# Optimization experiments

Measured on AMD Instinct MI355X. Metric: run time of the kernel, lower is better.

## Reference

```python
import jax, jax.numpy as jnp
import numpy as np

N_NODES = 50000
N_EDGES = 1600000
IN_DIM = 128
OUT_DIM = 64
HEADS = 4


def setup_inputs() -> dict:
    key = jax.random.key(0)
    k1, k2, k3, k4 = jax.random.split(key, 4)
    x = jax.random.normal(k1, (N_NODES, IN_DIM), dtype=jnp.float32)
    edge_index = jax.random.randint(k2, (2, N_EDGES), 0, N_NODES, dtype=jnp.int64)
    # W[h]: per-head linear weight (in_dim -> out_dim), no bias
    W = jax.random.normal(k3, (HEADS, IN_DIM, OUT_DIM), dtype=jnp.float32) * 0.1
    # a[h]: attention vector over concat([h_src, h_dst]) -> scalar, no bias
    a = jax.random.normal(k4, (HEADS, 2 * OUT_DIM), dtype=jnp.float32) * 0.1
    return {"x": x, "edge_index": edge_index, "W": W, "a": a}


def reference(x, edge_index, W, a):
    n_nodes = x.shape[0]
    out_dim = W.shape[2]
    src, dst = edge_index[0], edge_index[1]
    # per-head projection: [N, H, O]
    h = jnp.einsum('nf,hfo->nho', x, W)
    h_src = h[src]  # [E, H, O]
    h_dst = h[dst]  # [E, H, O]
    a_src, a_dst = a[:, :out_dim], a[:, out_dim:]  # split of concat weight
    # e = leaky_relu(a^T [h_src || h_dst]) per edge, per head: [E, H]
    e = jnp.einsum('eho,ho->eh', h_src, a_src) + jnp.einsum('eho,ho->eh', h_dst, a_dst)
    e = jax.nn.leaky_relu(e, negative_slope=0.01)
    # NOTE: faithful to source — softmax over ALL edges (dim=0), not per-dst
    alpha = jax.nn.softmax(e, axis=0)  # [E, H]
    msgs = h_src * alpha[:, :, None]  # [E, H, O]
    agg = jax.ops.segment_sum(msgs, dst, num_segments=n_nodes)  # [N, H, O]
    # concat heads along feature dim (head-major), matching torch.cat(out, dim=1)
    return agg.reshape(n_nodes, -1)
```

## Files before the change

### kernel.cpp

```cpp
#include <hip/hip_runtime.h>
#include <stdint.h>

#define N_NODES 50000
#define N_EDGES 1600000
#define IN_DIM  128
#define OUT_DIM 64
#define HEADS   4
#define HO      (HEADS*OUT_DIM)

typedef __attribute__((ext_vector_type(8))) short short8;
typedef __attribute__((ext_vector_type(8))) unsigned short bf16x8;
typedef __attribute__((ext_vector_type(4))) float f32x4;

__device__ __forceinline__ float lrelu(float v) {
    return v >= 0.f ? v : 0.01f * v;
}
__device__ __forceinline__ unsigned short f2bf(float f) {
    unsigned u = __float_as_uint(f);
    return (unsigned short)((u + 0x7FFFu + ((u >> 16) & 1u)) >> 16);
}
__device__ __forceinline__ float bf2f(unsigned short b) {
    return __uint_as_float(((unsigned)b) << 16);
}

__global__ __launch_bounds__(256) void k_prep_wt(
    const float* __restrict__ W, unsigned short* __restrict__ wt)
{
    int item = blockIdx.x * 256 + threadIdx.x;
    int n  = item >> 5;
    int k0 = (item & 31) * 4;
    int h = n >> 6, o = n & 63;
    const float* wp = &W[((size_t)h * IN_DIM + k0) * OUT_DIM + o];
    ushort4 u;
    u.x = f2bf(wp[0 * OUT_DIM]);
    u.y = f2bf(wp[1 * OUT_DIM]);
    u.z = f2bf(wp[2 * OUT_DIM]);
    u.w = f2bf(wp[3 * OUT_DIM]);
    *(ushort4*)&wt[(size_t)n * IN_DIM + k0] = u;
}

#define HIST_BLOCKS 1024
#define BM 64
#define GEMM_BLOCKS ((N_NODES + BM - 1) / BM)

__global__ __launch_bounds__(256) void k_gemm_hist(
    const float* __restrict__ x, const unsigned short* __restrict__ wt,
    const float* __restrict__ a, const int* __restrict__ edst,
    int* __restrict__ cnt, int* __restrict__ rank,
    unsigned short* __restrict__ hb, float* __restrict__ s_src, float* __restrict__ s_dst)
{
    extern __shared__ char smem[];

    if (blockIdx.x < HIST_BLOCKS) {
        const int stride = HIST_BLOCKS * 256;
        for (int e = blockIdx.x * 256 + threadIdx.x; e < N_EDGES; e += stride)
            rank[e] = atomicAdd(&cnt[edst[e]], 1);
        return;
    }

    char* Alds = smem;
    char* Blds = smem + 16384;

    const int tid  = threadIdx.x;
    const int wave = tid >> 6;
    const int lane = tid & 63;
    const int node0 = (blockIdx.x - HIST_BLOCKS) * BM;

    {
        #pragma unroll
        for (int j = 0; j < 4; ++j) {
            int o    = (j * 256 + tid) * 16;
            int row  = o >> 8;
            int fcol = (o & 255) >> 1;
            int node = node0 + row;
            const float* sp = x + (size_t)(node < N_NODES ? node : N_NODES - 1) * IN_DIM + fcol;
            float4 v0 = *(const float4*)sp;
            float4 v1 = *(const float4*)(sp + 4);
            bf16x8 u;
            u[0] = f2bf(v0.x); u[1] = f2bf(v0.y); u[2] = f2bf(v0.z); u[3] = f2bf(v0.w);
            u[4] = f2bf(v1.x); u[5] = f2bf(v1.y); u[6] = f2bf(v1.z); u[7] = f2bf(v1.w);
            int sw = o ^ (((o >> 8) & 7) << 4);
            *(bf16x8*)(Alds + sw) = u;
        }
    }
    {
        const char* wsrc = (const char*)wt;
        #pragma unroll
        for (int j = 0; j < 16; ++j) {
            int o = (j * 256 + tid) * 16;
            uint4 v = *(const uint4*)(wsrc + o);
            int sw = o ^ (((o >> 8) & 7) << 4);
            *(uint4*)(Blds + sw) = v;
        }
    }
    __syncthreads();

    const int wr0  = wave * 16;
    const int l15  = lane & 15;
    const int lhi  = lane >> 4;
    const int kxor = (lane & 7) << 4;

    short8 af[4];
    #pragma unroll
    for (int s = 0; s < 4; ++s)
        af[s] = *(const short8*)(Alds + (wr0 + l15) * 256 + ((s * 64 + lhi * 16) ^ kxor));

    f32x4 acc[16];
    #pragma unroll
    for (int nt = 0; nt < 16; ++nt) acc[nt] = (f32x4){0.f, 0.f, 0.f, 0.f};

    #pragma unroll
    for (int nt = 0; nt < 16; ++nt) {
        const char* bbase = Blds + (nt * 16 + l15) * 256;
        #pragma unroll
        for (int s = 0; s < 4; ++s) {
            short8 bf = *(const short8*)(bbase + ((s * 64 + lhi * 16) ^ kxor));
            acc[nt] = __builtin_amdgcn_mfma_f32_16x16x32_bf16(af[s], bf, acc[nt], 0, 0, 0);
        }
    }

    #pragma unroll
    for (int nt = 0; nt < 16; ++nt) {
        int col = nt * 16 + l15;
        #pragma unroll
        for (int r = 0; r < 4; ++r) {
            int node = node0 + wr0 + lhi * 4 + r;
            if (node < N_NODES)
                hb[(size_t)node * HO + col] = f2bf(acc[nt][r]);
        }
    }

    #pragma unroll
    for (int h = 0; h < 4; ++h) {
        float avs0 = a[h*128 +  0 + l15], avs1 = a[h*128 + 16 + l15];
        float avs2 = a[h*128 + 32 + l15], avs3 = a[h*128 + 48 + l15];
        float avd0 = a[h*128 + 64 + l15], avd1 = a[h*128 + 80 + l15];
        float avd2 = a[h*128 + 96 + l15], avd3 = a[h*128 + 112 + l15];
        #pragma unroll
        for (int r = 0; r < 4; ++r) {
            float vs = acc[4*h+0][r]*avs0 + acc[4*h+1][r]*avs1
                     + acc[4*h+2][r]*avs2 + acc[4*h+3][r]*avs3;
            float vd = acc[4*h+0][r]*avd0 + acc[4*h+1][r]*avd1
                     + acc[4*h+2][r]*avd2 + acc[4*h+3][r]*avd3;
            #pragma unroll
            for (int m = 8; m >= 1; m >>= 1) {
                vs += __shfl_xor(vs, m);
                vd += __shfl_xor(vd, m);
            }
            int node = node0 + wr0 + lhi * 4 + r;
            if (l15 == 0 && node < N_NODES) {
                s_src[node * HEADS + h] = vs;
                s_dst[node * HEADS + h] = vd;
            }
        }
    }
}

__global__ __launch_bounds__(1024) void k_mid(
    const int* __restrict__ cnt, int* __restrict__ row_start,
    const float* __restrict__ s_src, const float* __restrict__ s_dst,
    float* __restrict__ gmax)
{
    if (blockIdx.x == 0) {
        __shared__ int part[1024];
        const int t  = threadIdx.x;
        const int CH = (N_NODES + 1023) / 1024;
        const int lo = t * CH;
        const int hi = (lo + CH < N_NODES) ? lo + CH : N_NODES;

        int s = 0;
        for (int i = lo; i < hi; ++i) s += cnt[i];
        part[t] = s;
        __syncthreads();

        for (int off = 1; off < 1024; off <<= 1) {
            int v = (t >= off) ? part[t - off] : 0;
            __syncthreads();
            part[t] += v;
            __syncthreads();
        }

        int run = (t == 0) ? 0 : part[t - 1];
        for (int i = lo; i < hi; ++i) {
            row_start[i] = run;
            run += cnt[i];
        }
        if (t == 1023) row_start[N_NODES] = part[1023];
        return;
    }

    __shared__ float red[16][8];
    float4 ms = make_float4(-1e30f, -1e30f, -1e30f, -1e30f);
    float4 md = ms;
    for (int n = threadIdx.x; n < N_NODES; n += 1024) {
        float4 vs = ((const float4*)s_src)[n];
        float4 vd = ((const float4*)s_dst)[n];
        ms.x = fmaxf(ms.x, vs.x); ms.y = fmaxf(ms.y, vs.y);
        ms.z = fmaxf(ms.z, vs.z); ms.w = fmaxf(ms.w, vs.w);
        md.x = fmaxf(md.x, vd.x); md.y = fmaxf(md.y, vd.y);
        md.z = fmaxf(md.z, vd.z); md.w = fmaxf(md.w, vd.w);
    }
    #pragma unroll
    for (int m = 32; m >= 1; m >>= 1) {
        ms.x = fmaxf(ms.x, __shfl_xor(ms.x, m)); ms.y = fmaxf(ms.y, __shfl_xor(ms.y, m));
        ms.z = fmaxf(ms.z, __shfl_xor(ms.z, m)); ms.w = fmaxf(ms.w, __shfl_xor(ms.w, m));
        md.x = fmaxf(md.x, __shfl_xor(md.x, m)); md.y = fmaxf(md.y, __shfl_xor(md.y, m));
        md.z = fmaxf(md.z, __shfl_xor(md.z, m)); md.w = fmaxf(md.w, __shfl_xor(md.w, m));
    }
    const int w = threadIdx.x >> 6;
    if ((threadIdx.x & 63) == 0) {
        red[w][0] = ms.x; red[w][1] = ms.y; red[w][2] = ms.z; red[w][3] = ms.w;
        red[w][4] = md.x; red[w][5] = md.y; red[w][6] = md.z; red[w][7] = md.w;
    }
    __syncthreads();
    if (threadIdx.x < 8) {
        float m = red[0][threadIdx.x];
        #pragma unroll
        for (int k = 1; k < 16; ++k) m = fmaxf(m, red[k][threadIdx.x]);
        gmax[threadIdx.x] = m;
    }
}

#define BUCKET_BLOCKS 256
__global__ __launch_bounds__(256) void k_bucket(
    const int* __restrict__ esrc, const int* __restrict__ edst,
    const int* __restrict__ rank, const int* __restrict__ row_start,
    const float* __restrict__ s_src, const float* __restrict__ s_dst,
    const float* __restrict__ gmax,
    unsigned* __restrict__ rec, double* __restrict__ gsum)
{
    const float mx0 = lrelu(gmax[0] + gmax[4]);
    const float mx1 = lrelu(gmax[1] + gmax[5]);
    const float mx2 = lrelu(gmax[2] + gmax[6]);
    const float mx3 = lrelu(gmax[3] + gmax[7]);
    double a0 = 0.0, a1 = 0.0, a2 = 0.0, a3 = 0.0;
    const int stride = gridDim.x * blockDim.x;
    for (int e = blockIdx.x * blockDim.x + threadIdx.x; e < N_EDGES; e += stride) {
        int s = esrc[e], d = edst[e];
        int pos = row_start[d] + rank[e];
        float4 ss = *(const float4*)&s_src[s * HEADS];
        float4 sd = *(const float4*)&s_dst[d * HEADS];
        unsigned b0 = f2bf(__expf(lrelu(ss.x + sd.x) - mx0));
        unsigned b1 = f2bf(__expf(lrelu(ss.y + sd.y) - mx1));
        unsigned b2 = f2bf(__expf(lrelu(ss.z + sd.z) - mx2));
        unsigned b3 = f2bf(__expf(lrelu(ss.w + sd.w) - mx3));
        rec[(size_t)pos * 3 + 0] = (unsigned)s;
        rec[(size_t)pos * 3 + 1] = b0 | (b1 << 16);
        rec[(size_t)pos * 3 + 2] = b2 | (b3 << 16);
        a0 += (double)bf2f((unsigned short)b0);
        a1 += (double)bf2f((unsigned short)b1);
        a2 += (double)bf2f((unsigned short)b2);
        a3 += (double)bf2f((unsigned short)b3);
    }
    #pragma unroll
    for (int m = 32; m >= 1; m >>= 1) {
        a0 += __shfl_xor(a0, m); a1 += __shfl_xor(a1, m);
        a2 += __shfl_xor(a2, m); a3 += __shfl_xor(a3, m);
    }
    __shared__ double part[4][4];
    const int wave = threadIdx.x >> 6;
    if ((threadIdx.x & 63) == 0) {
        part[wave][0] = a0; part[wave][1] = a1; part[wave][2] = a2; part[wave][3] = a3;
    }
    __syncthreads();
    if (threadIdx.x < 4) {
        double t = part[0][threadIdx.x] + part[1][threadIdx.x]
                 + part[2][threadIdx.x] + part[3][threadIdx.x];
        atomicAdd(&gsum[(blockIdx.x & 7) * 4 + threadIdx.x], t);
    }
}

__global__ __launch_bounds__(256) void k_agg(
    const int* __restrict__ row_start, const unsigned* __restrict__ rec,
    const unsigned short* __restrict__ hb,
    const double* __restrict__ gsum, float* __restrict__ out)
{
    const int wid = (int)((blockIdx.x * 256u + threadIdx.x) >> 6);
    if (wid >= N_NODES) return;
    const int lane = threadIdx.x & 63;
    const int half = lane >> 5;
    const int l32  = lane & 31;
    const int head = l32 >> 3;
    const int og   = (l32 & 7) * 8;
    const int hoff = head * OUT_DIM + og;

    const int beg = row_start[wid];
    const int end = row_start[wid + 1];
    double gs = 0.0;
    #pragma unroll
    for (int r = 0; r < 8; ++r) gs += gsum[r * 4 + head];
    const float inv = (float)(1.0 / gs);

    float c0=0.f,c1=0.f,c2=0.f,c3=0.f,c4=0.f,c5=0.f,c6=0.f,c7=0.f;

    #define ALPHA(rc) bf2f((unsigned short)((head & 1)                          \
                        ? (((head & 2) ? (rc).z : (rc).y) >> 16)                \
                        : (((head & 2) ? (rc).z : (rc).y) & 0xFFFFu)))
    #define HROW(rc) (*(const bf16x8*)&hb[(size_t)(rc).x * HO + hoff])
    #define ACC(p,u)                                                            \
        { c0 = fmaf(p, bf2f((u)[0]), c0); c1 = fmaf(p, bf2f((u)[1]), c1);       \
          c2 = fmaf(p, bf2f((u)[2]), c2); c3 = fmaf(p, bf2f((u)[3]), c3);       \
          c4 = fmaf(p, bf2f((u)[4]), c4); c5 = fmaf(p, bf2f((u)[5]), c5);       \
          c6 = fmaf(p, bf2f((u)[6]), c6); c7 = fmaf(p, bf2f((u)[7]), c7); }

    int j = beg + half;
    for (; j + 14 < end; j += 16) {
        uint3 rA = *(const uint3*)&rec[(size_t)j * 3];
        uint3 rB = *(const uint3*)&rec[(size_t)(j + 2) * 3];
        uint3 rC = *(const uint3*)&rec[(size_t)(j + 4) * 3];
        uint3 rD = *(const uint3*)&rec[(size_t)(j + 6) * 3];
        uint3 rE = *(const uint3*)&rec[(size_t)(j + 8) * 3];
        uint3 rF = *(const uint3*)&rec[(size_t)(j + 10) * 3];
        uint3 rG = *(const uint3*)&rec[(size_t)(j + 12) * 3];
        uint3 rH = *(const uint3*)&rec[(size_t)(j + 14) * 3];
        bf16x8 uA = HROW(rA), uB = HROW(rB), uC = HROW(rC), uD = HROW(rD);
        bf16x8 uE = HROW(rE), uF = HROW(rF), uG = HROW(rG), uH = HROW(rH);
        float pA = ALPHA(rA), pB = ALPHA(rB), pC = ALPHA(rC), pD = ALPHA(rD);
        float pE = ALPHA(rE), pF = ALPHA(rF), pG = ALPHA(rG), pH = ALPHA(rH);
        ACC(pA,uA); ACC(pB,uB); ACC(pC,uC); ACC(pD,uD);
        ACC(pE,uE); ACC(pF,uF); ACC(pG,uG); ACC(pH,uH);
    }
    for (; j + 6 < end; j += 8) {
        uint3 rA = *(const uint3*)&rec[(size_t)j * 3];
        uint3 rB = *(const uint3*)&rec[(size_t)(j + 2) * 3];
        uint3 rC = *(const uint3*)&rec[(size_t)(j + 4) * 3];
        uint3 rD = *(const uint3*)&rec[(size_t)(j + 6) * 3];
        bf16x8 uA = HROW(rA), uB = HROW(rB), uC = HROW(rC), uD = HROW(rD);
        float pA = ALPHA(rA), pB = ALPHA(rB), pC = ALPHA(rC), pD = ALPHA(rD);
        ACC(pA,uA); ACC(pB,uB); ACC(pC,uC); ACC(pD,uD);
    }
    for (; j < end; j += 2) {
        uint3 rA = *(const uint3*)&rec[(size_t)j * 3];
        bf16x8 uA = HROW(rA);
        float pA = ALPHA(rA);
        ACC(pA,uA);
    }
    #undef ALPHA
    #undef HROW
    #undef ACC

    c0 += __shfl_xor(c0, 32); c1 += __shfl_xor(c1, 32);
    c2 += __shfl_xor(c2, 32); c3 += __shfl_xor(c3, 32);
    c4 += __shfl_xor(c4, 32); c5 += __shfl_xor(c5, 32);
    c6 += __shfl_xor(c6, 32); c7 += __shfl_xor(c7, 32);

    float4 v = half ? make_float4(c4 * inv, c5 * inv, c6 * inv, c7 * inv)
                    : make_float4(c0 * inv, c1 * inv, c2 * inv, c3 * inv);
    *(float4*)&out[(size_t)wid * HO + hoff + half * 4] = v;
}

extern "C" void kernel_launch(void* const* d_in, const int* in_sizes, int n_in,
                              void* d_out, int out_size, void* d_ws, size_t ws_size,
                              hipStream_t stream)
{
    const float* x    = (const float*)d_in[0];
    const int*   eidx = (const int*)d_in[1];
    const float* W    = (const float*)d_in[2];
    const float* a    = (const float*)d_in[3];
    float* out = (float*)d_out;

    unsigned short* hb = (unsigned short*)d_ws;
    unsigned short* wt = hb + (size_t)N_NODES * HO;
    float*    s_src    = (float*)(wt + (size_t)HO * IN_DIM);
    float*    s_dst    = s_src + (size_t)N_NODES * HEADS;
    double*   gsum     = (double*)(s_dst + (size_t)N_NODES * HEADS);
    float*    gmax     = (float*)(gsum + 32);
    int*      cnt      = (int*)(gmax + 8);
    int*      row_start = cnt + N_NODES;
    int*      rank     = row_start + (N_NODES + 2);
    unsigned* rec      = (unsigned*)(rank + N_EDGES);

    const int* esrc = eidx;
    const int* edst = eidx + N_EDGES;

    hipMemsetAsync(gsum, 0, 32 * sizeof(double) + 8 * sizeof(float) + N_NODES * sizeof(int),
                   stream);

    k_prep_wt<<<32, 256, 0, stream>>>(W, wt);
    k_gemm_hist<<<HIST_BLOCKS + GEMM_BLOCKS, 256, 81920, stream>>>(
        x, wt, a, edst, cnt, rank, hb, s_src, s_dst);
    k_mid<<<2, 1024, 0, stream>>>(cnt, row_start, s_src, s_dst, gmax);
    k_bucket<<<BUCKET_BLOCKS, 256, 0, stream>>>(
        esrc, edst, rank, row_start, s_src, s_dst, gmax, rec, gsum);
    k_agg<<<(N_NODES * 64 + 255) / 256, 256, 0, stream>>>(
        row_start, rec, hb, gsum, out);
}
```

Baseline: 318.7 us.

## Split edge records per head and slice aggregation by head-column block

The bucket kernel now writes four per-head edge record arrays of (src, alpha) pairs instead of one packed 12-byte record. The aggregation kernel launches eight blocks per group of four nodes, one per head/half-column slice. Each wave has 16 edge lanes and 4 column lanes that gather 32 columns, then reduce across lanes with shuffles. This aims to raise parallelism and shrink the per-wave working set, but it writes 32 bytes per edge instead of 12, re-reads row_start and the edge list 8 times per node, and drops the unrolled multi-load loop.

```diff
diff --git a/kernel.cpp b/kernel.cpp
--- a/kernel.cpp
+++ b/kernel.cpp
@@ -227,7 +227,7 @@
     const int* __restrict__ rank, const int* __restrict__ row_start,
     const float* __restrict__ s_src, const float* __restrict__ s_dst,
     const float* __restrict__ gmax,
-    unsigned* __restrict__ rec, double* __restrict__ gsum)
+    uint2* __restrict__ rech, double* __restrict__ gsum)
 {
     const float mx0 = lrelu(gmax[0] + gmax[4]);
     const float mx1 = lrelu(gmax[1] + gmax[5]);
@@ -244,9 +244,10 @@
         unsigned b1 = f2bf(__expf(lrelu(ss.y + sd.y) - mx1));
         unsigned b2 = f2bf(__expf(lrelu(ss.z + sd.z) - mx2));
         unsigned b3 = f2bf(__expf(lrelu(ss.w + sd.w) - mx3));
-        rec[(size_t)pos * 3 + 0] = (unsigned)s;
-        rec[(size_t)pos * 3 + 1] = b0 | (b1 << 16);
-        rec[(size_t)pos * 3 + 2] = b2 | (b3 << 16);
+        rech[pos]                       = make_uint2((unsigned)s, b0);
+        rech[N_EDGES + pos]             = make_uint2((unsigned)s, b1);
+        rech[2 * (size_t)N_EDGES + pos] = make_uint2((unsigned)s, b2);
+        rech[3 * (size_t)N_EDGES + pos] = make_uint2((unsigned)s, b3);
         a0 += (double)bf2f((unsigned short)b0);
         a1 += (double)bf2f((unsigned short)b1);
         a2 += (double)bf2f((unsigned short)b2);
@@ -271,21 +272,23 @@
 }
 
 __global__ __launch_bounds__(256) void k_agg(
-    const int* __restrict__ row_start, const unsigned* __restrict__ rec,
+    const int* __restrict__ row_start, const uint2* __restrict__ rech,
     const unsigned short* __restrict__ hb,
     const double* __restrict__ gsum, float* __restrict__ out)
 {
-    const int wid = (int)((blockIdx.x * 256u + threadIdx.x) >> 6);
+    const int slice = blockIdx.x & 7;
+    const int wid   = (blockIdx.x >> 3) * 4 + (threadIdx.x >> 6);
     if (wid >= N_NODES) return;
     const int lane = threadIdx.x & 63;
-    const int half = lane >> 5;
-    const int l32  = lane & 31;
-    const int head = l32 >> 3;
-    const int og   = (l32 & 7) * 8;
-    const int hoff = head * OUT_DIM + og;
+    const int eq   = lane >> 2;
+    const int cl   = lane & 3;
+    const int head = slice >> 1;
+    const int col  = head * OUT_DIM + (slice & 1) * 32 + cl * 8;
 
     const int beg = row_start[wid];
     const int end = row_start[wid + 1];
+    const uint2* rp = rech + (size_t)head * N_EDGES;
+
     double gs = 0.0;
     #pragma unroll
     for (int r = 0; r < 8; ++r) gs += gsum[r * 4 + head];
@@ -293,60 +296,29 @@
 
     float c0=0.f,c1=0.f,c2=0.f,c3=0.f,c4=0.f,c5=0.f,c6=0.f,c7=0.f;
 
-    #define ALPHA(rc) bf2f((unsigned short)((head & 1)                          \
-                        ? (((head & 2) ? (rc).z : (rc).y) >> 16)                \
-                        : (((head & 2) ? (rc).z : (rc).y) & 0xFFFFu)))
-    #define HROW(rc) (*(const bf16x8*)&hb[(size_t)(rc).x * HO + hoff])
-    #define ACC(p,u)                                                            \
-        { c0 = fmaf(p, bf2f((u)[0]), c0); c1 = fmaf(p, bf2f((u)[1]), c1);       \
-          c2 = fmaf(p, bf2f((u)[2]), c2); c3 = fmaf(p, bf2f((u)[3]), c3);       \
-          c4 = fmaf(p, bf2f((u)[4]), c4); c5 = fmaf(p, bf2f((u)[5]), c5);       \
-          c6 = fmaf(p, bf2f((u)[6]), c6); c7 = fmaf(p, bf2f((u)[7]), c7); }
-
-    int j = beg + half;
-    for (; j + 14 < end; j += 16) {
-        uint3 rA = *(const uint3*)&rec[(size_t)j * 3];
-        uint3 rB = *(const uint3*)&rec[(size_t)(j + 2) * 3];
-        uint3 rC = *(const uint3*)&rec[(size_t)(j + 4) * 3];
-        uint3 rD = *(const uint3*)&rec[(size_t)(j + 6) * 3];
-        uint3 rE = *(const uint3*)&rec[(size_t)(j + 8) * 3];
-        uint3 rF = *(const uint3*)&rec[(size_t)(j + 10) * 3];
-        uint3 rG = *(const uint3*)&rec[(size_t)(j + 12) * 3];
-        uint3 rH = *(const uint3*)&rec[(size_t)(j + 14) * 3];
-        bf16x8 uA = HROW(rA), uB = HROW(rB), uC = HROW(rC), uD = HROW(rD);
-        bf16x8 uE = HROW(rE), uF = HROW(rF), uG = HROW(rG), uH = HROW(rH);
-        float pA = ALPHA(rA), pB = ALPHA(rB), pC = ALPHA(rC), pD = ALPHA(rD);
-        float pE = ALPHA(rE), pF = ALPHA(rF), pG = ALPHA(rG), pH = ALPHA(rH);
-        ACC(pA,uA); ACC(pB,uB); ACC(pC,uC); ACC(pD,uD);
-        ACC(pE,uE); ACC(pF,uF); ACC(pG,uG); ACC(pH,uH);
-    }
-    for (; j + 6 < end; j += 8) {
-        uint3 rA = *(const uint3*)&rec[(size_t)j * 3];
-        uint3 rB = *(const uint3*)&rec[(size_t)(j + 2) * 3];
-        uint3 rC = *(const uint3*)&rec[(size_t)(j + 4) * 3];
-        uint3 rD = *(const uint3*)&rec[(size_t)(j + 6) * 3];
-        bf16x8 uA = HROW(rA), uB = HROW(rB), uC = HROW(rC), uD = HROW(rD);
-        float pA = ALPHA(rA), pB = ALPHA(rB), pC = ALPHA(rC), pD = ALPHA(rD);
-        ACC(pA,uA); ACC(pB,uB); ACC(pC,uC); ACC(pD,uD);
-    }
-    for (; j < end; j += 2) {
-        uint3 rA = *(const uint3*)&rec[(size_t)j * 3];
-        bf16x8 uA = HROW(rA);
-        float pA = ALPHA(rA);
-        ACC(pA,uA);
-    }
-    #undef ALPHA
-    #undef HROW
-    #undef ACC
-
-    c0 += __shfl_xor(c0, 32); c1 += __shfl_xor(c1, 32);
-    c2 += __shfl_xor(c2, 32); c3 += __shfl_xor(c3, 32);
-    c4 += __shfl_xor(c4, 32); c5 += __shfl_xor(c5, 32);
-    c6 += __shfl_xor(c6, 32); c7 += __shfl_xor(c7, 32);
-
-    float4 v = half ? make_float4(c4 * inv, c5 * inv, c6 * inv, c7 * inv)
-                    : make_float4(c0 * inv, c1 * inv, c2 * inv, c3 * inv);
-    *(float4*)&out[(size_t)wid * HO + hoff + half * 4] = v;
+    for (int j = beg + eq; j < end; j += 16) {
+        uint2 r = rp[j];
+        float p = bf2f((unsigned short)r.y);
+        bf16x8 u = *(const bf16x8*)&hb[(size_t)r.x * HO + col];
+        c0 = fmaf(p, bf2f(u[0]), c0); c1 = fmaf(p, bf2f(u[1]), c1);
+        c2 = fmaf(p, bf2f(u[2]), c2); c3 = fmaf(p, bf2f(u[3]), c3);
+        c4 = fmaf(p, bf2f(u[4]), c4); c5 = fmaf(p, bf2f(u[5]), c5);
+        c6 = fmaf(p, bf2f(u[6]), c6); c7 = fmaf(p, bf2f(u[7]), c7);
+    }
+
+    #pragma unroll
+    for (int m = 4; m <= 32; m <<= 1) {
+        c0 += __shfl_xor(c0, m); c1 += __shfl_xor(c1, m);
+        c2 += __shfl_xor(c2, m); c3 += __shfl_xor(c3, m);
+        c4 += __shfl_xor(c4, m); c5 += __shfl_xor(c5, m);
+        c6 += __shfl_xor(c6, m); c7 += __shfl_xor(c7, m);
+    }
+
+    if (eq == 0) {
+        float* op = &out[(size_t)wid * HO + col];
+        *(float4*)op       = make_float4(c0 * inv, c1 * inv, c2 * inv, c3 * inv);
+        *(float4*)(op + 4) = make_float4(c4 * inv, c5 * inv, c6 * inv, c7 * inv);
+    }
 }
 
 extern "C" void kernel_launch(void* const* d_in, const int* in_sizes, int n_in,
@@ -368,7 +340,7 @@
     int*      cnt      = (int*)(gmax + 8);
     int*      row_start = cnt + N_NODES;
     int*      rank     = row_start + (N_NODES + 2);
-    unsigned* rec      = (unsigned*)(rank + N_EDGES);
+    uint2*    rech     = (uint2*)(rank + N_EDGES);
 
     const int* esrc = eidx;
     const int* edst = eidx + N_EDGES;
@@ -381,7 +353,7 @@
         x, wt, a, edst, cnt, rank, hb, s_src, s_dst);
     k_mid<<<2, 1024, 0, stream>>>(cnt, row_start, s_src, s_dst, gmax);
     k_bucket<<<BUCKET_BLOCKS, 256, 0, stream>>>(
-        esrc, edst, rank, row_start, s_src, s_dst, gmax, rec, gsum);
-    k_agg<<<(N_NODES * 64 + 255) / 256, 256, 0, stream>>>(
-        row_start, rec, hb, gsum, out);
-}
+        esrc, edst, rank, row_start, s_src, s_dst, gmax, rech, gsum);
+    k_agg<<<((N_NODES + 3) / 4) * 8, 256, 0, stream>>>(
+        row_start, rech, hb, gsum, out);
+}
```

New measurement: 439.7 us. 38.0% more time.

## Stage projected rows through LDS for coalesced stores; simplify aggregation loop

Applied to the files above, without the earlier changes.

The projection kernel now writes its bf16 results into swizzled shared memory and then copies whole 512-byte rows to global memory with 16-byte vector stores, replacing scattered 2-byte stores. This targets uncoalesced write traffic for the projected features, at the cost of two barriers and reuse of the LDS tile buffer. The aggregation kernel drops its 16-edge unrolled loop and merges the load, alpha extraction and FMAs per edge into one macro. That change trades memory-level parallelism for lower register pressure.

```diff
diff --git a/kernel.cpp b/kernel.cpp
--- a/kernel.cpp
+++ b/kernel.cpp
@@ -116,17 +116,6 @@
         for (int s = 0; s < 4; ++s) {
             short8 bf = *(const short8*)(bbase + ((s * 64 + lhi * 16) ^ kxor));
             acc[nt] = __builtin_amdgcn_mfma_f32_16x16x32_bf16(af[s], bf, acc[nt], 0, 0, 0);
-        }
-    }
-
-    #pragma unroll
-    for (int nt = 0; nt < 16; ++nt) {
-        int col = nt * 16 + l15;
-        #pragma unroll
-        for (int r = 0; r < 4; ++r) {
-            int node = node0 + wr0 + lhi * 4 + r;
-            if (node < N_NODES)
-                hb[(size_t)node * HO + col] = f2bf(acc[nt][r]);
         }
     }
 
@@ -152,6 +141,31 @@
                 s_src[node * HEADS + h] = vs;
                 s_dst[node * HEADS + h] = vd;
             }
+        }
+    }
+
+    __syncthreads();
+    #pragma unroll
+    for (int nt = 0; nt < 16; ++nt) {
+        int col = nt * 16 + l15;
+        #pragma unroll
+        for (int r = 0; r < 4; ++r) {
+            int row  = wr0 + lhi * 4 + r;
+            int byte = (row * 512 + col * 2) ^ ((row & 7) << 4);
+            *(unsigned short*)(smem + byte) = f2bf(acc[nt][r]);
+        }
+    }
+    __syncthreads();
+    {
+        char* hdst = (char*)hb + (size_t)node0 * 512;
+        #pragma unroll
+        for (int k = 0; k < 8; ++k) {
+            int i    = k * 256 + tid;
+            int row  = i >> 5;
+            int byte = (row * 512 + (i & 31) * 16) ^ ((row & 7) << 4);
+            uint4 v  = *(const uint4*)(smem + byte);
+            if (node0 + row < N_NODES)
+                *(uint4*)(hdst + (size_t)i * 16) = v;
         }
     }
 }
@@ -293,51 +307,31 @@
 
     float c0=0.f,c1=0.f,c2=0.f,c3=0.f,c4=0.f,c5=0.f,c6=0.f,c7=0.f;
 
-    #define ALPHA(rc) bf2f((unsigned short)((head & 1)                          \
-                        ? (((head & 2) ? (rc).z : (rc).y) >> 16)                \
-                        : (((head & 2) ? (rc).z : (rc).y) & 0xFFFFu)))
-    #define HROW(rc) (*(const bf16x8*)&hb[(size_t)(rc).x * HO + hoff])
-    #define ACC(p,u)                                                            \
-        { c0 = fmaf(p, bf2f((u)[0]), c0); c1 = fmaf(p, bf2f((u)[1]), c1);       \
-          c2 = fmaf(p, bf2f((u)[2]), c2); c3 = fmaf(p, bf2f((u)[3]), c3);       \
-          c4 = fmaf(p, bf2f((u)[4]), c4); c5 = fmaf(p, bf2f((u)[5]), c5);       \
-          c6 = fmaf(p, bf2f((u)[6]), c6); c7 = fmaf(p, bf2f((u)[7]), c7); }
+    #define EDGE(rc)                                                            \
+        {                                                                       \
+            unsigned aw = (head & 2) ? (rc).z : (rc).y;                         \
+            float p = bf2f((unsigned short)((head & 1) ? (aw >> 16)             \
+                                                       : (aw & 0xFFFFu)));      \
+            bf16x8 u = *(const bf16x8*)&hb[(size_t)(rc).x * HO + hoff];         \
+            c0 = fmaf(p, bf2f(u[0]), c0); c1 = fmaf(p, bf2f(u[1]), c1);         \
+            c2 = fmaf(p, bf2f(u[2]), c2); c3 = fmaf(p, bf2f(u[3]), c3);         \
+            c4 = fmaf(p, bf2f(u[4]), c4); c5 = fmaf(p, bf2f(u[5]), c5);         \
+            c6 = fmaf(p, bf2f(u[6]), c6); c7 = fmaf(p, bf2f(u[7]), c7);         \
+        }
 
     int j = beg + half;
-    for (; j + 14 < end; j += 16) {
-        uint3 rA = *(const uint3*)&rec[(size_t)j * 3];
-        uint3 rB = *(const uint3*)&rec[(size_t)(j + 2) * 3];
-        uint3 rC = *(const uint3*)&rec[(size_t)(j + 4) * 3];
-        uint3 rD = *(const uint3*)&rec[(size_t)(j + 6) * 3];
-        uint3 rE = *(const uint3*)&rec[(size_t)(j + 8) * 3];
-        uint3 rF = *(const uint3*)&rec[(size_t)(j + 10) * 3];
-        uint3 rG = *(const uint3*)&rec[(size_t)(j + 12) * 3];
-        uint3 rH = *(const uint3*)&rec[(size_t)(j + 14) * 3];
-        bf16x8 uA = HROW(rA), uB = HROW(rB), uC = HROW(rC), uD = HROW(rD);
-        bf16x8 uE = HROW(rE), uF = HROW(rF), uG = HROW(rG), uH = HROW(rH);
-        float pA = ALPHA(rA), pB = ALPHA(rB), pC = ALPHA(rC), pD = ALPHA(rD);
-        float pE = ALPHA(rE), pF = ALPHA(rF), pG = ALPHA(rG), pH = ALPHA(rH);
-        ACC(pA,uA); ACC(pB,uB); ACC(pC,uC); ACC(pD,uD);
-        ACC(pE,uE); ACC(pF,uF); ACC(pG,uG); ACC(pH,uH);
-    }
     for (; j + 6 < end; j += 8) {
         uint3 rA = *(const uint3*)&rec[(size_t)j * 3];
         uint3 rB = *(const uint3*)&rec[(size_t)(j + 2) * 3];
         uint3 rC = *(const uint3*)&rec[(size_t)(j + 4) * 3];
         uint3 rD = *(const uint3*)&rec[(size_t)(j + 6) * 3];
-        bf16x8 uA = HROW(rA), uB = HROW(rB), uC = HROW(rC), uD = HROW(rD);
-        float pA = ALPHA(rA), pB = ALPHA(rB), pC = ALPHA(rC), pD = ALPHA(rD);
-        ACC(pA,uA); ACC(pB,uB); ACC(pC,uC); ACC(pD,uD);
+        EDGE(rA); EDGE(rB); EDGE(rC); EDGE(rD);
     }
     for (; j < end; j += 2) {
         uint3 rA = *(const uint3*)&rec[(size_t)j * 3];
-        bf16x8 uA = HROW(rA);
-        float pA = ALPHA(rA);
-        ACC(pA,uA);
-    }
-    #undef ALPHA
-    #undef HROW
-    #undef ACC
+        EDGE(rA);
+    }
+    #undef EDGE
 
     c0 += __shfl_xor(c0, 32); c1 += __shfl_xor(c1, 32);
     c2 += __shfl_xor(c2, 32); c3 += __shfl_xor(c3, 32);
```

Result: no change. 318.2 us (-0.2%).
